# Performance work log

Measured on AMD Instinct MI355X. Metric: run time of the kernel, lower is better.

The kernel has to match this reference:

```python
import jax, jax.numpy as jnp
import numpy as np

N = 50000   # nodes
E = 800000  # edges
R = 2000    # relations
F = 128     # node_F / rel_F
DEPTH = 2
FD = F * (DEPTH + 1)  # 384
P = 64      # proxy rows
EPS = 1e-12


def setup_inputs() -> dict:
    key = jax.random.key(0)
    ks = jax.random.split(key, 16)
    inp = {
        'ent_emb': jax.random.normal(ks[0], (N, F), jnp.float32) * 0.05,
        'rel_emb': jax.random.normal(ks[1], (R, F), jnp.float32) * 0.05,
        'edge_src': jax.random.randint(ks[2], (E,), 0, N, jnp.int32),
        'edge_dst': jax.random.randint(ks[3], (E,), 0, N, jnp.int32),
        'edge_rel': jax.random.randint(ks[4], (E,), 0, R, jnp.int32),
        'attn_e': jax.random.normal(ks[5], (DEPTH, F, 1), jnp.float32) * 0.1,
        'gate_e': jax.random.normal(ks[6], (FD, FD), jnp.float32) * 0.05,
        'proxy_e': jax.random.normal(ks[7], (P, FD), jnp.float32) * 0.1,
        'bias_e': jnp.zeros((1, FD), jnp.float32),
        'attn_r': jax.random.normal(ks[8], (DEPTH, F, 1), jnp.float32) * 0.1,
        'gate_r': jax.random.normal(ks[9], (FD, FD), jnp.float32) * 0.05,
        'proxy_r': jax.random.normal(ks[10], (P, FD), jnp.float32) * 0.1,
        'bias_r': jnp.zeros((1, FD), jnp.float32),
    }
    return inp


def _l2norm(x, axis=-1):
    n = jnp.sqrt(jnp.sum(x * x, axis=axis, keepdims=True))
    return x / jnp.maximum(n, EPS)


def _dual(features, rel_emb, edge_src, edge_dst, edge_rel,
          attn_kernels, gate_kernel, proxy, bias):
    feats = jnp.tanh(features)            # [N, F]
    outs = [feats]
    for l in range(DEPTH):
        # per-edge relation feature (mean over relation set == gather here), L2-normalized
        rels_sum = _l2norm(rel_emb[edge_rel])          # [E, F]
        neighs = feats[edge_src]                       # [E, F]
        # Householder reflection of neighbor features across relation direction
        dot = jnp.sum(neighs * rels_sum, axis=1, keepdims=True)
        neighs = neighs - 2.0 * dot * rels_sum
        # edge_softmax normalized by dst
        att1 = jnp.squeeze(rels_sum @ attn_kernels[l], -1)   # [E]
        seg_max = jax.ops.segment_max(att1, edge_dst, num_segments=N)
        ex = jnp.exp(att1 - seg_max[edge_dst])
        seg_sum = jax.ops.segment_sum(ex, edge_dst, num_segments=N)
        att = ex / seg_sum[edge_dst]
        # weighted scatter-sum aggregation
        agg = jax.ops.segment_sum(neighs * att[:, None], edge_dst, num_segments=N)
        feats = jnp.tanh(agg)
        outs.append(feats)
    outputs = jnp.concatenate(outs, axis=1)            # [N, FD]
    proxy_att = jax.nn.softmax(_l2norm(outputs) @ _l2norm(proxy).T, axis=-1)  # [N, P]
    proxy_feature = outputs - proxy_att @ proxy
    gate = jax.nn.sigmoid(proxy_feature @ gate_kernel + bias)
    return gate * outputs + (1.0 - gate) * proxy_feature


def reference(ent_emb, rel_emb, edge_src, edge_dst, edge_rel,
              attn_e, gate_e, proxy_e, bias_e,
              attn_r, gate_r, proxy_r, bias_r):
    # initial features: mean of neighbor entity / relation embeddings per dst node
    deg = jax.ops.segment_sum(jnp.ones((E,), jnp.float32), edge_dst, num_segments=N)
    deg = jnp.maximum(deg, 1.0)[:, None]
    ent_feature = jax.ops.segment_sum(ent_emb[edge_src], edge_dst, num_segments=N) / deg
    rel_feature = jax.ops.segment_sum(rel_emb[edge_rel], edge_dst, num_segments=N) / deg
    out_ent = _dual(ent_feature, rel_emb, edge_src, edge_dst, edge_rel,
                    attn_e, gate_e, proxy_e, bias_e)
    out_rel = _dual(rel_feature, rel_emb, edge_src, edge_dst, edge_rel,
                    attn_r, gate_r, proxy_r, bias_r)
    return jnp.concatenate((out_ent, out_rel), axis=-1)  # [N, 2*FD]
```

## Files before the change

### kernel.cpp

```cpp
#include <hip/hip_runtime.h>
#include <math.h>


#define NN    50000
#define NE    800000
#define NR    2000
#define FF    128
#define FDIM  384
#define OD    768
#define PP    64
#define NEPS  1e-12f
#define NPB   32
#define FSTR  388
#define ASTR  68
#define NBLK  49

typedef unsigned int u32;
typedef unsigned short u16;
typedef __attribute__((ext_vector_type(8))) short bf16x8;
typedef __attribute__((ext_vector_type(8))) _Float16 f16x8;
typedef __attribute__((ext_vector_type(4))) float f32x4;

__device__ int   g_rowptr[NN + 1];
__device__ int   g_cnt[NN];
__device__ int   g_bsum[64];
__device__ u32   g_csr[NE];
__device__ float g_relnorm[NR * FF];
__device__ float2 g_ew[2 * NR];
__device__ __attribute__((aligned(16))) _Float16 g_hh[2][NN][256];
__device__ __attribute__((aligned(16))) _Float16 g_ent16[NN * FF];
__device__ __attribute__((aligned(16))) u16 g_wt_hi[2 * FDIM * FDIM];
__device__ __attribute__((aligned(16))) u16 g_wt_lo[2 * FDIM * FDIM];
__device__ __attribute__((aligned(16))) u16 g_pxn_hi[2 * PP * FDIM];
__device__ __attribute__((aligned(16))) u16 g_pxn_lo[2 * PP * FDIM];
__device__ __attribute__((aligned(16))) u16 g_pxT_hi[2 * FDIM * PP];
__device__ __attribute__((aligned(16))) u16 g_pxT_lo[2 * FDIM * PP];

__device__ __forceinline__ float wsum64(float v) {
#pragma unroll
    for (int m = 32; m > 0; m >>= 1) v += __shfl_xor(v, m, 64);
    return v;
}
__device__ __forceinline__ void red16x2(float& a, float& b) {
#pragma unroll
    for (int m = 1; m < 16; m <<= 1) {
        float ta = __shfl_xor(a, m, 64);
        float tb = __shfl_xor(b, m, 64);
        a += ta; b += tb;
    }
}

__device__ __forceinline__ u32 pack_bf(float f) {
    u32 x = __float_as_uint(f);
    u32 hr = (x + 0x7FFFu + ((x >> 16) & 1u)) & 0xFFFF0000u;
    float res = f - __uint_as_float(hr);
    u32 y = __float_as_uint(res);
    u32 lr = (y + 0x7FFFu + ((y >> 16) & 1u)) >> 16;
    return hr | lr;
}
__device__ __forceinline__ float unpack_bf(u32 pk) {
    return __uint_as_float(pk & 0xFFFF0000u) + __uint_as_float(pk << 16);
}

__device__ __forceinline__ void load_afrag(const u32* p, bf16x8& ah, bf16x8& al) {
    u32 q[8];
    *reinterpret_cast<float4*>(q)     = *reinterpret_cast<const float4*>(p);
    *reinterpret_cast<float4*>(q + 4) = *reinterpret_cast<const float4*>(p + 4);
    union { u32 u[4]; bf16x8 v; } H, L;
#pragma unroll
    for (int j = 0; j < 4; j++) {
        H.u[j] = __builtin_amdgcn_perm(q[2 * j + 1], q[2 * j], 0x07060302u);
        L.u[j] = __builtin_amdgcn_perm(q[2 * j + 1], q[2 * j], 0x05040100u);
    }
    ah = H.v; al = L.v;
}

__global__ __launch_bounds__(256) void k_zero() {
    int i = blockIdx.x * 256 + threadIdx.x;
    if (i < NN) g_cnt[i] = 0;
}

__global__ __launch_bounds__(256) void k_prep_rel(
    const float* __restrict__ rel_emb, const float* __restrict__ attn_e,
    const float* __restrict__ attn_r) {
    int wave = threadIdx.x >> 6, lane = threadIdx.x & 63;
    int r = blockIdx.x * 4 + wave;
    if (r >= NR) return;
    float2 v = *(const float2*)(rel_emb + r * FF + 2 * lane);
    float ss = wsum64(v.x * v.x + v.y * v.y);
    float inv = 1.f / fmaxf(sqrtf(ss), NEPS);
    float rn0 = v.x * inv, rn1 = v.y * inv;
    *(float2*)(g_relnorm + r * FF + 2 * lane) = make_float2(rn0, rn1);
#pragma unroll
    for (int t = 0; t < 4; t++) {
        const float* av = ((t < 2) ? attn_e : attn_r) + (t & 1) * FF + 2 * lane;
        float d = wsum64(rn0 * av[0] + rn1 * av[1]);
        if (lane == 0) ((float*)&g_ew[(t & 1) * NR + r])[t >> 1] = expf(d);
    }
}

__global__ __launch_bounds__(256) void k_prep_ent(const float* __restrict__ ent_emb) {
    int i = (blockIdx.x * 256 + threadIdx.x) * 8;
    if (i >= NN * FF) return;
    float4 a = *(const float4*)(ent_emb + i);
    float4 b = *(const float4*)(ent_emb + i + 4);
    f16x8 h;
    h[0] = (_Float16)a.x; h[1] = (_Float16)a.y; h[2] = (_Float16)a.z; h[3] = (_Float16)a.w;
    h[4] = (_Float16)b.x; h[5] = (_Float16)b.y; h[6] = (_Float16)b.z; h[7] = (_Float16)b.w;
    *(f16x8*)(g_ent16 + i) = h;
}

__global__ __launch_bounds__(256) void k_prep_proxy(
    const float* __restrict__ proxy_e, const float* __restrict__ proxy_r) {
    int wave = threadIdx.x >> 6, lane = threadIdx.x & 63;
    int row = blockIdx.x * 4 + wave;
    if (row >= 2 * PP) return;
    int d = row >> 6, p = row & 63;
    const float* pr = ((d == 0) ? proxy_e : proxy_r) + p * FDIM;
    float v[6];
    float ss = 0.f;
#pragma unroll
    for (int j = 0; j < 6; j++) {
        v[j] = pr[lane + 64 * j];
        ss += v[j] * v[j];
    }
    ss = wsum64(ss);
    float inv = 1.f / fmaxf(sqrtf(ss), NEPS);
#pragma unroll
    for (int j = 0; j < 6; j++) {
        int k = lane + 64 * j;
        u32 pn = pack_bf(v[j] * inv);
        g_pxn_hi[(d * PP + p) * FDIM + k] = (u16)(pn >> 16);
        g_pxn_lo[(d * PP + p) * FDIM + k] = (u16)(pn & 0xFFFFu);
        u32 pt = pack_bf(v[j]);
        g_pxT_hi[(d * FDIM + k) * PP + p] = (u16)(pt >> 16);
        g_pxT_lo[(d * FDIM + k) * PP + p] = (u16)(pt & 0xFFFFu);
    }
}

__global__ __launch_bounds__(256) void k_prep_wt(
    const float* __restrict__ gate_e, const float* __restrict__ gate_r) {
    int idx = blockIdx.x * 256 + threadIdx.x;
    if (idx >= 2 * FDIM * FDIM) return;
    int d = idx / (FDIM * FDIM);
    int rem = idx - d * (FDIM * FDIM);
    int k = rem / FDIM;
    int f = rem - k * FDIM;
    float wv = (d ? gate_r : gate_e)[k * FDIM + f];
    u32 pk = pack_bf(wv);
    g_wt_hi[(d * FDIM + f) * FDIM + k] = (u16)(pk >> 16);
    g_wt_lo[(d * FDIM + f) * FDIM + k] = (u16)(pk & 0xFFFFu);
}

__global__ __launch_bounds__(256) void k_count(const int* __restrict__ dst) {
    int e = blockIdx.x * 256 + threadIdx.x;
    if (e < NE) atomicAdd(&g_cnt[dst[e]], 1);
}

__global__ __launch_bounds__(1024) void k_scan1() {
    __shared__ int s[1024];
    int b = blockIdx.x, tid = threadIdx.x;
    int i = b * 1024 + tid;
    int v = (i < NN) ? g_cnt[i] : 0;
    s[tid] = v;
    __syncthreads();
    for (int off = 1; off < 1024; off <<= 1) {
        int t = (tid >= off) ? s[tid - off] : 0;
        __syncthreads();
        s[tid] += t;
        __syncthreads();
    }
    if (i < NN) {
        g_rowptr[i] = s[tid] - v;
        g_cnt[i] = 0;
    }
    if (tid == 1023) g_bsum[b] = s[1023];
}
__global__ __launch_bounds__(64) void k_scan2() {
    int lane = threadIdx.x;
    int v = (lane < NBLK) ? g_bsum[lane] : 0;
#pragma unroll
    for (int off = 1; off < 64; off <<= 1) {
        int t = __shfl_up(v, off, 64);
        if (lane >= off) v += t;
    }
    if (lane < NBLK) g_bsum[lane] = v;
    if (lane == 0) g_rowptr[NN] = NE;
}
__global__ __launch_bounds__(1024) void k_scan3() {
    int b = blockIdx.x;
    if (b == 0) return;
    int i = b * 1024 + threadIdx.x;
    if (i < NN) g_rowptr[i] += g_bsum[b - 1];
}

__global__ __launch_bounds__(256) void k_fill(
    const int* __restrict__ src, const int* __restrict__ dst,
    const int* __restrict__ rel) {
    int e = blockIdx.x * 256 + threadIdx.x;
    if (e >= NE) return;
    int d = dst[e];
    int pos = atomicAdd(&g_cnt[d], 1);
    g_csr[g_rowptr[d] + pos] = ((u32)src[e] << 16) | (u32)rel[e];
}

__global__ __launch_bounds__(256) void k_init(
    const float* __restrict__ rel_emb, float* __restrict__ out) {
    int wave = threadIdx.x >> 6, lane = threadIdx.x & 63;
    int n = blockIdx.x * 4 + wave;
    if (n >= NN) return;
    int g16 = lane >> 4, li = lane & 15;
    int s0 = g_rowptr[n], s1 = g_rowptr[n + 1];
    float ae[8], ar[8];
#pragma unroll
    for (int i = 0; i < 8; i++) { ae[i] = 0.f; ar[i] = 0.f; }
    for (int idx = s0; idx < s1; idx += 4) {
        int e = idx + g16;
        if (e < s1) {
            u32 pk = g_csr[e];
            int s = (int)(pk >> 16), r = (int)(pk & 0xFFFFu);
            f16x8 ev = *(const f16x8*)(g_ent16 + (size_t)s * FF + 8 * li);
            const float* rp = rel_emb + (size_t)r * FF + 8 * li;
            float4 r0 = *(const float4*)rp, r1 = *(const float4*)(rp + 4);
            float rv[8] = {r0.x, r0.y, r0.z, r0.w, r1.x, r1.y, r1.z, r1.w};
#pragma unroll
            for (int i = 0; i < 8; i++) {
                ae[i] += (float)ev[i];
                ar[i] += rv[i];
            }
        }
    }
#pragma unroll
    for (int mk = 16; mk < 64; mk <<= 1)
#pragma unroll
        for (int i = 0; i < 8; i++) {
            ae[i] += __shfl_xor(ae[i], mk, 64);
            ar[i] += __shfl_xor(ar[i], mk, 64);
        }
    float invd = 1.f / (float)max(s1 - s0, 1);
    if (g16 == 0) {
        float fe[8], fr[8];
#pragma unroll
        for (int i = 0; i < 8; i++) {
            fe[i] = tanhf(ae[i] * invd);
            fr[i] = tanhf(ar[i] * invd);
        }
        float* oe = out + (size_t)n * OD + 8 * li;
        float* orp = out + (size_t)n * OD + FDIM + 8 * li;
        *(float4*)oe = make_float4(fe[0], fe[1], fe[2], fe[3]);
        *(float4*)(oe + 4) = make_float4(fe[4], fe[5], fe[6], fe[7]);
        *(float4*)orp = make_float4(fr[0], fr[1], fr[2], fr[3]);
        *(float4*)(orp + 4) = make_float4(fr[4], fr[5], fr[6], fr[7]);
        _Float16* hh = &g_hh[0][n][0];
        f16x8 he, hr;
#pragma unroll
        for (int i = 0; i < 8; i++) { he[i] = (_Float16)fe[i]; hr[i] = (_Float16)fr[i]; }
        *(f16x8*)(hh + 8 * li) = he;
        *(f16x8*)(hh + 128 + 8 * li) = hr;
    }
}

__global__ __launch_bounds__(256) void k_layer(float* buf, int layer) {
    int wave = threadIdx.x >> 6, lane = threadIdx.x & 63;
    int n = blockIdx.x * 4 + wave;
    if (n >= NN) return;
    int g16 = lane >> 4, li = lane & 15;
    int bo_e = (layer + 1) * FF;
    int bo_r = FDIM + (layer + 1) * FF;
    const float2* ew = g_ew + layer * NR;
    const _Float16* hs = &g_hh[layer][0][0];
    int s0 = g_rowptr[n], s1 = g_rowptr[n + 1];
    if (s1 == s0) {
        if (g16 == 0) {
            float* oe = buf + (size_t)n * OD + bo_e + 8 * li;
            float* orp = buf + (size_t)n * OD + bo_r + 8 * li;
            *(float4*)oe = make_float4(0.f, 0.f, 0.f, 0.f);
            *(float4*)(oe + 4) = make_float4(0.f, 0.f, 0.f, 0.f);
            *(float4*)orp = make_float4(0.f, 0.f, 0.f, 0.f);
            *(float4*)(orp + 4) = make_float4(0.f, 0.f, 0.f, 0.f);
            if (layer == 0) {
                _Float16* hh = &g_hh[1][n][0];
                f16x8 z = (f16x8)(_Float16)0.f;
                *(f16x8*)(hh + 8 * li) = z;
                *(f16x8*)(hh + 128 + 8 * li) = z;
            }
        }
        return;
    }
    float ae[8], ar[8];
#pragma unroll
    for (int i = 0; i < 8; i++) { ae[i] = 0.f; ar[i] = 0.f; }
    float wse = 0.f, wsr = 0.f;
    for (int idx = s0; idx < s1; idx += 4) {
        int e = idx + g16;
        bool act = e < s1;
        u32 pk = g_csr[act ? e : s0];
        int s = (int)(pk >> 16), r = (int)(pk & 0xFFFFu);
        const _Float16* hrow = hs + (size_t)s * 256;
        f16x8 hev = *(const f16x8*)(hrow + 8 * li);
        f16x8 hrv = *(const f16x8*)(hrow + 128 + 8 * li);
        const float* rp = g_relnorm + (size_t)r * FF + 8 * li;
        float4 rn0 = *(const float4*)rp;
        float4 rn1 = *(const float4*)(rp + 4);
        float rnv[8] = {rn0.x, rn0.y, rn0.z, rn0.w, rn1.x, rn1.y, rn1.z, rn1.w};
        float he[8], hr[8];
#pragma unroll
        for (int i = 0; i < 8; i++) { he[i] = (float)hev[i]; hr[i] = (float)hrv[i]; }
        float de = 0.f, dr = 0.f;
#pragma unroll
        for (int i = 0; i < 8; i++) {
            de = fmaf(he[i], rnv[i], de);
            dr = fmaf(hr[i], rnv[i], dr);
        }
        red16x2(de, dr);
        float2 wv = act ? ew[r] : make_float2(0.f, 0.f);
        wse += wv.x; wsr += wv.y;
        float te = -2.f * de, tr = -2.f * dr;
#pragma unroll
        for (int i = 0; i < 8; i++) {
            ae[i] = fmaf(wv.x, fmaf(te, rnv[i], he[i]), ae[i]);
            ar[i] = fmaf(wv.y, fmaf(tr, rnv[i], hr[i]), ar[i]);
        }
    }
#pragma unroll
    for (int mk = 16; mk < 64; mk <<= 1) {
#pragma unroll
        for (int i = 0; i < 8; i++) {
            ae[i] += __shfl_xor(ae[i], mk, 64);
            ar[i] += __shfl_xor(ar[i], mk, 64);
        }
        wse += __shfl_xor(wse, mk, 64);
        wsr += __shfl_xor(wsr, mk, 64);
    }
    float ive = 1.f / wse, ivr = 1.f / wsr;
    if (g16 == 0) {
        float fe[8], fr[8];
#pragma unroll
        for (int i = 0; i < 8; i++) {
            fe[i] = tanhf(ae[i] * ive);
            fr[i] = tanhf(ar[i] * ivr);
        }
        float* oe = buf + (size_t)n * OD + bo_e + 8 * li;
        float* orp = buf + (size_t)n * OD + bo_r + 8 * li;
        *(float4*)oe = make_float4(fe[0], fe[1], fe[2], fe[3]);
        *(float4*)(oe + 4) = make_float4(fe[4], fe[5], fe[6], fe[7]);
        *(float4*)orp = make_float4(fr[0], fr[1], fr[2], fr[3]);
        *(float4*)(orp + 4) = make_float4(fr[4], fr[5], fr[6], fr[7]);
        if (layer == 0) {
            _Float16* hh = &g_hh[1][n][0];
            f16x8 he16, hr16;
#pragma unroll
            for (int i = 0; i < 8; i++) { he16[i] = (_Float16)fe[i]; hr16[i] = (_Float16)fr[i]; }
            *(f16x8*)(hh + 8 * li) = he16;
            *(f16x8*)(hh + 128 + 8 * li) = hr16;
        }
    }
}

__global__ __launch_bounds__(256, 2) void k_pg(
    float* out, const float* __restrict__ bias_e,
    const float* __restrict__ bias_r) {
    __shared__ __attribute__((aligned(16))) u32 o_pk[NPB * FSTR];
    __shared__ __attribute__((aligned(16))) u32 att_pk[NPB * ASTR];
    __shared__ float invn_s[NPB];
    int tid = threadIdx.x;
    int lane = tid & 63, w = tid >> 6;
    int c = lane & 15, kg = lane >> 4;
    int n0 = blockIdx.x * NPB, dual = blockIdx.y;
    int dual_off = dual * FDIM;
    const float* bias = dual ? bias_r : bias_e;
    const u16* wt_h = g_wt_hi + dual * (FDIM * FDIM);
    const u16* wt_l = g_wt_lo + dual * (FDIM * FDIM);
    const u16* pn_h = g_pxn_hi + dual * (PP * FDIM);
    const u16* pn_l = g_pxn_lo + dual * (PP * FDIM);
    const u16* pt_h = g_pxT_hi + dual * (FDIM * PP);
    const u16* pt_l = g_pxT_lo + dual * (FDIM * PP);

    {
        float2 v[8][3];
        float ss[8];
#pragma unroll
        for (int j = 0; j < 8; j++) {
            int n = w + 4 * j;
            int gn = n0 + n;
            if (gn < NN) {
                const float* rp = out + (size_t)gn * OD + dual_off;
#pragma unroll
                for (int q = 0; q < 3; q++) v[j][q] = *(const float2*)(rp + 2 * (lane + 64 * q));
            } else {
                v[j][0] = v[j][1] = v[j][2] = make_float2(0.f, 0.f);
            }
            ss[j] = v[j][0].x * v[j][0].x + v[j][0].y * v[j][0].y
                  + v[j][1].x * v[j][1].x + v[j][1].y * v[j][1].y
                  + v[j][2].x * v[j][2].x + v[j][2].y * v[j][2].y;
        }
#pragma unroll
        for (int m = 32; m > 0; m >>= 1)
#pragma unroll
            for (int j = 0; j < 8; j++) ss[j] += __shfl_xor(ss[j], m, 64);
#pragma unroll
        for (int j = 0; j < 8; j++) {
            int n = w + 4 * j;
            if (lane == 0) invn_s[n] = 1.f / fmaxf(sqrtf(ss[j]), NEPS);
#pragma unroll
            for (int q = 0; q < 3; q++) {
                uint2 pr;
                pr.x = pack_bf(v[j][q].x);
                pr.y = pack_bf(v[j][q].y);
                *(uint2*)(o_pk + n * FSTR + 2 * (lane + 64 * q)) = pr;
            }
        }
    }
    __syncthreads();

    {
        f32x4 lacc[2] = {{0.f,0.f,0.f,0.f},{0.f,0.f,0.f,0.f}};
        const u16* bh_p = pn_h + (16 * w + c) * FDIM;
        const u16* bl_p = pn_l + (16 * w + c) * FDIM;
#pragma unroll 2
        for (int ks = 0; ks < 12; ks++) {
            int kb = 32 * ks + 8 * kg;
            bf16x8 bh = *(const bf16x8*)(bh_p + kb);
            bf16x8 bl = *(const bf16x8*)(bl_p + kb);
#pragma unroll
            for (int m = 0; m < 2; m++) {
                bf16x8 ah, al;
                load_afrag(o_pk + (16 * m + c) * FSTR + kb, ah, al);
                lacc[m] = __builtin_amdgcn_mfma_f32_16x16x32_bf16(ah, bh, lacc[m], 0, 0, 0);
                lacc[m] = __builtin_amdgcn_mfma_f32_16x16x32_bf16(al, bh, lacc[m], 0, 0, 0);
                lacc[m] = __builtin_amdgcn_mfma_f32_16x16x32_bf16(ah, bl, lacc[m], 0, 0, 0);
            }
        }
#pragma unroll
        for (int m = 0; m < 2; m++)
#pragma unroll
            for (int i = 0; i < 4; i++) {
                int n = 16 * m + 4 * kg + i;
                att_pk[n * ASTR + 16 * w + c] = __float_as_uint(lacc[m][i] * invn_s[n]);
            }
    }
    __syncthreads();

    {
        float ev[8], sv[8];
#pragma unroll
        for (int j = 0; j < 8; j++) {
            int n = w + 4 * j;
            ev[j] = expf(__uint_as_float(att_pk[n * ASTR + lane]));
            sv[j] = ev[j];
        }
#pragma unroll
        for (int m = 32; m > 0; m >>= 1)
#pragma unroll
            for (int j = 0; j < 8; j++) sv[j] += __shfl_xor(sv[j], m, 64);
#pragma unroll
        for (int j = 0; j < 8; j++) {
            int n = w + 4 * j;
            att_pk[n * ASTR + lane] = pack_bf(ev[j] / sv[j]);
        }
    }
    __syncthreads();

    f32x4 pacc[2][6];
#pragma unroll
    for (int m = 0; m < 2; m++)
#pragma unroll
        for (int t = 0; t < 6; t++) pacc[m][t] = (f32x4){0.f, 0.f, 0.f, 0.f};
    {
        bf16x8 aah[2][2], aal[2][2];
#pragma unroll
        for (int m = 0; m < 2; m++) {
            load_afrag(att_pk + (16 * m + c) * ASTR + 8 * kg, aah[m][0], aal[m][0]);
            load_afrag(att_pk + (16 * m + c) * ASTR + 32 + 8 * kg, aah[m][1], aal[m][1]);
        }
#pragma unroll
        for (int t = 0; t < 6; t++) {
            int f = 96 * w + 16 * t + c;
            const u16* bh0 = pt_h + f * PP;
            const u16* bl0 = pt_l + f * PP;
            bf16x8 b0h = *(const bf16x8*)(bh0 + 8 * kg);
            bf16x8 b0l = *(const bf16x8*)(bl0 + 8 * kg);
            bf16x8 b1h = *(const bf16x8*)(bh0 + 32 + 8 * kg);
            bf16x8 b1l = *(const bf16x8*)(bl0 + 32 + 8 * kg);
#pragma unroll
            for (int m = 0; m < 2; m++) {
                pacc[m][t] = __builtin_amdgcn_mfma_f32_16x16x32_bf16(aah[m][0], b0h, pacc[m][t], 0, 0, 0);
                pacc[m][t] = __builtin_amdgcn_mfma_f32_16x16x32_bf16(aal[m][0], b0h, pacc[m][t], 0, 0, 0);
                pacc[m][t] = __builtin_amdgcn_mfma_f32_16x16x32_bf16(aah[m][0], b0l, pacc[m][t], 0, 0, 0);
                pacc[m][t] = __builtin_amdgcn_mfma_f32_16x16x32_bf16(aah[m][1], b1h, pacc[m][t], 0, 0, 0);
                pacc[m][t] = __builtin_amdgcn_mfma_f32_16x16x32_bf16(aal[m][1], b1h, pacc[m][t], 0, 0, 0);
                pacc[m][t] = __builtin_amdgcn_mfma_f32_16x16x32_bf16(aah[m][1], b1l, pacc[m][t], 0, 0, 0);
            }
        }
#pragma unroll
        for (int t = 0; t < 6; t++) {
            int f = 96 * w + 16 * t + c;
#pragma unroll
            for (int m = 0; m < 2; m++)
#pragma unroll
                for (int i = 0; i < 4; i++) {
                    int n = 16 * m + 4 * kg + i;
                    u32 pk = o_pk[n * FSTR + f];
                    o_pk[n * FSTR + f] = pack_bf(unpack_bf(pk) - pacc[m][t][i]);
                }
        }
    }
    __syncthreads();

    f32x4 gacc[2][6];
#pragma unroll
    for (int m = 0; m < 2; m++)
#pragma unroll
        for (int t = 0; t < 6; t++) gacc[m][t] = (f32x4){0.f, 0.f, 0.f, 0.f};
    {
        const u16* wtw_h = wt_h + (96 * w + c) * FDIM;
        const u16* wtw_l = wt_l + (96 * w + c) * FDIM;
#pragma unroll 2
        for (int ks = 0; ks < 12; ks++) {
            int kb = 32 * ks + 8 * kg;
            bf16x8 bhv[6], blv[6];
#pragma unroll
            for (int t = 0; t < 6; t++) {
                bhv[t] = *(const bf16x8*)(wtw_h + t * 16 * FDIM + kb);
                blv[t] = *(const bf16x8*)(wtw_l + t * 16 * FDIM + kb);
            }
            bf16x8 ah[2], al[2];
#pragma unroll
            for (int m = 0; m < 2; m++)
                load_afrag(o_pk + (16 * m + c) * FSTR + kb, ah[m], al[m]);
#pragma unroll
            for (int t = 0; t < 6; t++)
#pragma unroll
                for (int m = 0; m < 2; m++) {
                    gacc[m][t] = __builtin_amdgcn_mfma_f32_16x16x32_bf16(ah[m], bhv[t], gacc[m][t], 0, 0, 0);
                    gacc[m][t] = __builtin_amdgcn_mfma_f32_16x16x32_bf16(al[m], bhv[t], gacc[m][t], 0, 0, 0);
                    gacc[m][t] = __builtin_amdgcn_mfma_f32_16x16x32_bf16(ah[m], blv[t], gacc[m][t], 0, 0, 0);
                }
        }
    }

#pragma unroll
    for (int t = 0; t < 6; t++) {
        int fcol = 96 * w + 16 * t + c;
        float b = bias[fcol];
#pragma unroll
        for (int m = 0; m < 2; m++)
#pragma unroll
            for (int i = 0; i < 4; i++) {
                int n = 16 * m + 4 * kg + i;
                int gn = n0 + n;
                if (gn < NN) {
                    float lin = gacc[m][t][i] + b;
                    float gt = 1.f / (1.f + expf(-lin));
                    float pv = unpack_bf(o_pk[n * FSTR + fcol]);
                    float ov = pv + pacc[m][t][i];
                    out[(size_t)gn * OD + dual_off + fcol] = gt * ov + (1.f - gt) * pv;
                }
            }
    }
}

extern "C" void kernel_launch(void* const* d_in, const int* in_sizes, int n_in,
                              void* d_out, int out_size, void* d_ws, size_t ws_size,
                              hipStream_t stream) {
    const float* ent_emb = (const float*)d_in[0];
    const float* rel_emb = (const float*)d_in[1];
    const int* e_src     = (const int*)d_in[2];
    const int* e_dst     = (const int*)d_in[3];
    const int* e_rel     = (const int*)d_in[4];
    const float* attn_e  = (const float*)d_in[5];
    const float* gate_e  = (const float*)d_in[6];
    const float* proxy_e = (const float*)d_in[7];
    const float* bias_e  = (const float*)d_in[8];
    const float* attn_r  = (const float*)d_in[9];
    const float* gate_r  = (const float*)d_in[10];
    const float* proxy_r = (const float*)d_in[11];
    const float* bias_r  = (const float*)d_in[12];
    float* out = (float*)d_out;
    (void)d_ws; (void)ws_size; (void)in_sizes; (void)n_in; (void)out_size;

    k_zero<<<(NN + 255) / 256, 256, 0, stream>>>();
    k_prep_rel<<<NR / 4, 256, 0, stream>>>(rel_emb, attn_e, attn_r);
    k_prep_ent<<<(NN * FF / 8 + 255) / 256, 256, 0, stream>>>(ent_emb);
    k_prep_proxy<<<32, 256, 0, stream>>>(proxy_e, proxy_r);
    k_prep_wt<<<(2 * FDIM * FDIM + 255) / 256, 256, 0, stream>>>(gate_e, gate_r);
    k_count<<<(NE + 255) / 256, 256, 0, stream>>>(e_dst);
    k_scan1<<<NBLK, 1024, 0, stream>>>();
    k_scan2<<<1, 64, 0, stream>>>();
    k_scan3<<<NBLK, 1024, 0, stream>>>();
    k_fill<<<(NE + 255) / 256, 256, 0, stream>>>(e_src, e_dst, e_rel);
    k_init<<<NN / 4, 256, 0, stream>>>(rel_emb, out);
    k_layer<<<NN / 4, 256, 0, stream>>>(out, 0);
    k_layer<<<NN / 4, 256, 0, stream>>>(out, 1);
    k_pg<<<dim3((NN + NPB - 1) / NPB, 2), 256, 0, stream>>>(out, bias_e, bias_r);
}
```

Baseline: 866.1 us.

## Restructure proxy-gate kernel into independent per-wave 16-row tiles without block barriers

Each wave now processes its own 16 nodes across all 384 output columns, replacing the shared 32-row block tile and its __syncthreads phases with per-wave scratch only. Rows are streamed straight from global memory into MFMA fragments. The row norm and the proxy softmax are done with shuffles inside the wave. The final combine is rewritten algebraically as outputs minus (1-gate) times the proxy term, recomputing the attention-times-proxy product to keep register use down. In exchange, each wave reloads the full gate weight and proxy matrices, doubling weight traffic per row, and register pressure rises sharply from the large accumulator arrays.

Result: slower. 1.885 ms (+117.6%).

```diff
diff --git a/kernel.cpp b/kernel.cpp
--- a/kernel.cpp
+++ b/kernel.cpp
@@ -10,10 +10,9 @@
 #define OD    768
 #define PP    64
 #define NEPS  1e-12f
-#define NPB   32
-#define FSTR  388
-#define ASTR  68
 #define NBLK  49
+#define SCRW  68
+#define TSTR  36
 
 typedef unsigned int u32;
 typedef unsigned short u16;
@@ -62,17 +61,20 @@
     return __uint_as_float(pk & 0xFFFF0000u) + __uint_as_float(pk << 16);
 }
 
+__device__ __forceinline__ void split_frag(const u32 q[8], bf16x8& ah, bf16x8& al) {
+    union { u32 u[4]; bf16x8 v; } H, L;
+#pragma unroll
+    for (int j = 0; j < 4; j++) {
+        H.u[j] = __builtin_amdgcn_perm(q[2 * j + 1], q[2 * j], 0x07060302u);
+        L.u[j] = __builtin_amdgcn_perm(q[2 * j + 1], q[2 * j], 0x05040100u);
+    }
+    ah = H.v; al = L.v;
+}
 __device__ __forceinline__ void load_afrag(const u32* p, bf16x8& ah, bf16x8& al) {
     u32 q[8];
     *reinterpret_cast<float4*>(q)     = *reinterpret_cast<const float4*>(p);
     *reinterpret_cast<float4*>(q + 4) = *reinterpret_cast<const float4*>(p + 4);
-    union { u32 u[4]; bf16x8 v; } H, L;
-#pragma unroll
-    for (int j = 0; j < 4; j++) {
-        H.u[j] = __builtin_amdgcn_perm(q[2 * j + 1], q[2 * j], 0x07060302u);
-        L.u[j] = __builtin_amdgcn_perm(q[2 * j + 1], q[2 * j], 0x05040100u);
-    }
-    ah = H.v; al = L.v;
+    split_frag(q, ah, al);
 }
 
 __global__ __launch_bounds__(256) void k_zero() {
@@ -360,14 +362,14 @@
 __global__ __launch_bounds__(256, 2) void k_pg(
     float* out, const float* __restrict__ bias_e,
     const float* __restrict__ bias_r) {
-    __shared__ __attribute__((aligned(16))) u32 o_pk[NPB * FSTR];
-    __shared__ __attribute__((aligned(16))) u32 att_pk[NPB * ASTR];
-    __shared__ float invn_s[NPB];
+    __shared__ __attribute__((aligned(16))) u32 scr[4][16 * SCRW + 16 * TSTR];
     int tid = threadIdx.x;
     int lane = tid & 63, w = tid >> 6;
     int c = lane & 15, kg = lane >> 4;
-    int n0 = blockIdx.x * NPB, dual = blockIdx.y;
-    int dual_off = dual * FDIM;
+    int dual = blockIdx.y;
+    int n0w = blockIdx.x * 64 + w * 16;
+    if (n0w >= NN) return;
+    int doff = dual * FDIM;
     const float* bias = dual ? bias_r : bias_e;
     const u16* wt_h = g_wt_hi + dual * (FDIM * FDIM);
     const u16* wt_l = g_wt_lo + dual * (FDIM * FDIM);
@@ -375,188 +377,157 @@
     const u16* pn_l = g_pxn_lo + dual * (PP * FDIM);
     const u16* pt_h = g_pxT_hi + dual * (FDIM * PP);
     const u16* pt_l = g_pxT_lo + dual * (FDIM * PP);
-
-    {
-        float2 v[8][3];
-        float ss[8];
+    u32* scrA = scr[w];
+    float* scrT = (float*)(scr[w] + 16 * SCRW);
+    const float* orow = out + (size_t)(n0w + c) * OD + doff;
+
+    float ss = 0.f;
+    f32x4 lacc[4];
+#pragma unroll
+    for (int pt = 0; pt < 4; pt++) lacc[pt] = (f32x4){0.f, 0.f, 0.f, 0.f};
+#pragma unroll
+    for (int ks = 0; ks < 12; ks++) {
+        int kb = 32 * ks + 8 * kg;
+        float4 f0 = *(const float4*)(orow + kb);
+        float4 f1 = *(const float4*)(orow + kb + 4);
+        float fv[8] = {f0.x, f0.y, f0.z, f0.w, f1.x, f1.y, f1.z, f1.w};
+        u32 pk[8];
 #pragma unroll
         for (int j = 0; j < 8; j++) {
-            int n = w + 4 * j;
-            int gn = n0 + n;
-            if (gn < NN) {
-                const float* rp = out + (size_t)gn * OD + dual_off;
-#pragma unroll
-                for (int q = 0; q < 3; q++) v[j][q] = *(const float2*)(rp + 2 * (lane + 64 * q));
-            } else {
-                v[j][0] = v[j][1] = v[j][2] = make_float2(0.f, 0.f);
-            }
-            ss[j] = v[j][0].x * v[j][0].x + v[j][0].y * v[j][0].y
-                  + v[j][1].x * v[j][1].x + v[j][1].y * v[j][1].y
-                  + v[j][2].x * v[j][2].x + v[j][2].y * v[j][2].y;
-        }
-#pragma unroll
-        for (int m = 32; m > 0; m >>= 1)
-#pragma unroll
-            for (int j = 0; j < 8; j++) ss[j] += __shfl_xor(ss[j], m, 64);
-#pragma unroll
-        for (int j = 0; j < 8; j++) {
-            int n = w + 4 * j;
-            if (lane == 0) invn_s[n] = 1.f / fmaxf(sqrtf(ss[j]), NEPS);
-#pragma unroll
-            for (int q = 0; q < 3; q++) {
-                uint2 pr;
-                pr.x = pack_bf(v[j][q].x);
-                pr.y = pack_bf(v[j][q].y);
-                *(uint2*)(o_pk + n * FSTR + 2 * (lane + 64 * q)) = pr;
-            }
-        }
-    }
-    __syncthreads();
-
-    {
-        f32x4 lacc[2] = {{0.f,0.f,0.f,0.f},{0.f,0.f,0.f,0.f}};
-        const u16* bh_p = pn_h + (16 * w + c) * FDIM;
-        const u16* bl_p = pn_l + (16 * w + c) * FDIM;
+            ss = fmaf(fv[j], fv[j], ss);
+            pk[j] = pack_bf(fv[j]);
+        }
+        bf16x8 ah, al;
+        split_frag(pk, ah, al);
+#pragma unroll
+        for (int pt = 0; pt < 4; pt++) {
+            bf16x8 bh = *(const bf16x8*)(pn_h + (16 * pt + c) * FDIM + kb);
+            bf16x8 bl = *(const bf16x8*)(pn_l + (16 * pt + c) * FDIM + kb);
+            lacc[pt] = __builtin_amdgcn_mfma_f32_16x16x32_bf16(ah, bh, lacc[pt], 0, 0, 0);
+            lacc[pt] = __builtin_amdgcn_mfma_f32_16x16x32_bf16(al, bh, lacc[pt], 0, 0, 0);
+            lacc[pt] = __builtin_amdgcn_mfma_f32_16x16x32_bf16(ah, bl, lacc[pt], 0, 0, 0);
+        }
+    }
+    ss += __shfl_xor(ss, 16, 64);
+    ss += __shfl_xor(ss, 32, 64);
+    float invn = 1.f / fmaxf(sqrtf(ss), NEPS);
+
+    float ev[4][4], den[4] = {0.f, 0.f, 0.f, 0.f};
+#pragma unroll
+    for (int i = 0; i < 4; i++) {
+        float ivi = __shfl(invn, 4 * kg + i, 64);
+#pragma unroll
+        for (int pt = 0; pt < 4; pt++) {
+            float e = expf(lacc[pt][i] * ivi);
+            ev[pt][i] = e;
+            den[i] += e;
+        }
+    }
+#pragma unroll
+    for (int m = 1; m < 16; m <<= 1)
+#pragma unroll
+        for (int i = 0; i < 4; i++) den[i] += __shfl_xor(den[i], m, 64);
+#pragma unroll
+    for (int i = 0; i < 4; i++) {
+        float rd = 1.f / den[i];
+#pragma unroll
+        for (int pt = 0; pt < 4; pt++)
+            scrA[(4 * kg + i) * SCRW + 16 * pt + c] = pack_bf(ev[pt][i] * rd);
+    }
+    bf16x8 aah0, aal0, aah1, aal1;
+    load_afrag(scrA + c * SCRW + 8 * kg, aah0, aal0);
+    load_afrag(scrA + c * SCRW + 32 + 8 * kg, aah1, aal1);
+
+    f32x4 pacc[24];
+#pragma unroll
+    for (int t = 0; t < 24; t++) pacc[t] = (f32x4){0.f, 0.f, 0.f, 0.f};
 #pragma unroll 2
-        for (int ks = 0; ks < 12; ks++) {
-            int kb = 32 * ks + 8 * kg;
-            bf16x8 bh = *(const bf16x8*)(bh_p + kb);
-            bf16x8 bl = *(const bf16x8*)(bl_p + kb);
-#pragma unroll
-            for (int m = 0; m < 2; m++) {
-                bf16x8 ah, al;
-                load_afrag(o_pk + (16 * m + c) * FSTR + kb, ah, al);
-                lacc[m] = __builtin_amdgcn_mfma_f32_16x16x32_bf16(ah, bh, lacc[m], 0, 0, 0);
-                lacc[m] = __builtin_amdgcn_mfma_f32_16x16x32_bf16(al, bh, lacc[m], 0, 0, 0);
-                lacc[m] = __builtin_amdgcn_mfma_f32_16x16x32_bf16(ah, bl, lacc[m], 0, 0, 0);
-            }
-        }
-#pragma unroll
-        for (int m = 0; m < 2; m++)
-#pragma unroll
-            for (int i = 0; i < 4; i++) {
-                int n = 16 * m + 4 * kg + i;
-                att_pk[n * ASTR + 16 * w + c] = __float_as_uint(lacc[m][i] * invn_s[n]);
-            }
-    }
-    __syncthreads();
-
-    {
-        float ev[8], sv[8];
-#pragma unroll
-        for (int j = 0; j < 8; j++) {
-            int n = w + 4 * j;
-            ev[j] = expf(__uint_as_float(att_pk[n * ASTR + lane]));
-            sv[j] = ev[j];
-        }
-#pragma unroll
-        for (int m = 32; m > 0; m >>= 1)
-#pragma unroll
-            for (int j = 0; j < 8; j++) sv[j] += __shfl_xor(sv[j], m, 64);
-#pragma unroll
-        for (int j = 0; j < 8; j++) {
-            int n = w + 4 * j;
-            att_pk[n * ASTR + lane] = pack_bf(ev[j] / sv[j]);
-        }
-    }
-    __syncthreads();
-
-    f32x4 pacc[2][6];
-#pragma unroll
-    for (int m = 0; m < 2; m++)
-#pragma unroll
-        for (int t = 0; t < 6; t++) pacc[m][t] = (f32x4){0.f, 0.f, 0.f, 0.f};
-    {
-        bf16x8 aah[2][2], aal[2][2];
-#pragma unroll
-        for (int m = 0; m < 2; m++) {
-            load_afrag(att_pk + (16 * m + c) * ASTR + 8 * kg, aah[m][0], aal[m][0]);
-            load_afrag(att_pk + (16 * m + c) * ASTR + 32 + 8 * kg, aah[m][1], aal[m][1]);
-        }
-#pragma unroll
-        for (int t = 0; t < 6; t++) {
-            int f = 96 * w + 16 * t + c;
-            const u16* bh0 = pt_h + f * PP;
-            const u16* bl0 = pt_l + f * PP;
-            bf16x8 b0h = *(const bf16x8*)(bh0 + 8 * kg);
-            bf16x8 b0l = *(const bf16x8*)(bl0 + 8 * kg);
-            bf16x8 b1h = *(const bf16x8*)(bh0 + 32 + 8 * kg);
-            bf16x8 b1l = *(const bf16x8*)(bl0 + 32 + 8 * kg);
-#pragma unroll
-            for (int m = 0; m < 2; m++) {
-                pacc[m][t] = __builtin_amdgcn_mfma_f32_16x16x32_bf16(aah[m][0], b0h, pacc[m][t], 0, 0, 0);
-                pacc[m][t] = __builtin_amdgcn_mfma_f32_16x16x32_bf16(aal[m][0], b0h, pacc[m][t], 0, 0, 0);
-                pacc[m][t] = __builtin_amdgcn_mfma_f32_16x16x32_bf16(aah[m][0], b0l, pacc[m][t], 0, 0, 0);
-                pacc[m][t] = __builtin_amdgcn_mfma_f32_16x16x32_bf16(aah[m][1], b1h, pacc[m][t], 0, 0, 0);
-                pacc[m][t] = __builtin_amdgcn_mfma_f32_16x16x32_bf16(aal[m][1], b1h, pacc[m][t], 0, 0, 0);
-                pacc[m][t] = __builtin_amdgcn_mfma_f32_16x16x32_bf16(aah[m][1], b1l, pacc[m][t], 0, 0, 0);
-            }
-        }
-#pragma unroll
-        for (int t = 0; t < 6; t++) {
-            int f = 96 * w + 16 * t + c;
-#pragma unroll
-            for (int m = 0; m < 2; m++)
-#pragma unroll
-                for (int i = 0; i < 4; i++) {
-                    int n = 16 * m + 4 * kg + i;
-                    u32 pk = o_pk[n * FSTR + f];
-                    o_pk[n * FSTR + f] = pack_bf(unpack_bf(pk) - pacc[m][t][i]);
-                }
-        }
-    }
-    __syncthreads();
-
-    f32x4 gacc[2][6];
-#pragma unroll
-    for (int m = 0; m < 2; m++)
-#pragma unroll
-        for (int t = 0; t < 6; t++) gacc[m][t] = (f32x4){0.f, 0.f, 0.f, 0.f};
-    {
-        const u16* wtw_h = wt_h + (96 * w + c) * FDIM;
-        const u16* wtw_l = wt_l + (96 * w + c) * FDIM;
+    for (int t = 0; t < 24; t++) {
+        const u16* bh0 = pt_h + (16 * t + c) * PP;
+        const u16* bl0 = pt_l + (16 * t + c) * PP;
+        bf16x8 b0h = *(const bf16x8*)(bh0 + 8 * kg);
+        bf16x8 b0l = *(const bf16x8*)(bl0 + 8 * kg);
+        bf16x8 b1h = *(const bf16x8*)(bh0 + 32 + 8 * kg);
+        bf16x8 b1l = *(const bf16x8*)(bl0 + 32 + 8 * kg);
+        pacc[t] = __builtin_amdgcn_mfma_f32_16x16x32_bf16(aah0, b0h, pacc[t], 0, 0, 0);
+        pacc[t] = __builtin_amdgcn_mfma_f32_16x16x32_bf16(aal0, b0h, pacc[t], 0, 0, 0);
+        pacc[t] = __builtin_amdgcn_mfma_f32_16x16x32_bf16(aah0, b0l, pacc[t], 0, 0, 0);
+        pacc[t] = __builtin_amdgcn_mfma_f32_16x16x32_bf16(aah1, b1h, pacc[t], 0, 0, 0);
+        pacc[t] = __builtin_amdgcn_mfma_f32_16x16x32_bf16(aal1, b1h, pacc[t], 0, 0, 0);
+        pacc[t] = __builtin_amdgcn_mfma_f32_16x16x32_bf16(aah1, b1l, pacc[t], 0, 0, 0);
+    }
+
+    bf16x8 pfh[12], pfl[12];
+#pragma unroll
+    for (int ks = 0; ks < 12; ks++) {
+#pragma unroll
+        for (int u = 0; u < 2; u++) {
+            int t = 2 * ks + u;
+#pragma unroll
+            for (int i = 0; i < 4; i++)
+                scrT[(4 * kg + i) * TSTR + 16 * u + c] = pacc[t][i];
+        }
+        int kb = 32 * ks + 8 * kg;
+        float4 o0 = *(const float4*)(orow + kb);
+        float4 o1 = *(const float4*)(orow + kb + 4);
+        float ofv[8] = {o0.x, o0.y, o0.z, o0.w, o1.x, o1.y, o1.z, o1.w};
+        float4 p0 = *(const float4*)(scrT + c * TSTR + 8 * kg);
+        float4 p1 = *(const float4*)(scrT + c * TSTR + 8 * kg + 4);
+        float pfv[8] = {p0.x, p0.y, p0.z, p0.w, p1.x, p1.y, p1.z, p1.w};
+        u32 pk[8];
+#pragma unroll
+        for (int j = 0; j < 8; j++) pk[j] = pack_bf(ofv[j] - pfv[j]);
+        split_frag(pk, pfh[ks], pfl[ks]);
+    }
+
+    f32x4 lin[24];
+#pragma unroll
+    for (int t = 0; t < 24; t++) lin[t] = (f32x4){0.f, 0.f, 0.f, 0.f};
+#pragma unroll
+    for (int ks = 0; ks < 12; ks++) {
+        int kb = 32 * ks + 8 * kg;
+        bf16x8 ah = pfh[ks], al = pfl[ks];
+#pragma unroll 4
+        for (int t = 0; t < 24; t++) {
+            bf16x8 bh = *(const bf16x8*)(wt_h + (16 * t + c) * FDIM + kb);
+            bf16x8 bl = *(const bf16x8*)(wt_l + (16 * t + c) * FDIM + kb);
+            lin[t] = __builtin_amdgcn_mfma_f32_16x16x32_bf16(ah, bh, lin[t], 0, 0, 0);
+            lin[t] = __builtin_amdgcn_mfma_f32_16x16x32_bf16(al, bh, lin[t], 0, 0, 0);
+            lin[t] = __builtin_amdgcn_mfma_f32_16x16x32_bf16(ah, bl, lin[t], 0, 0, 0);
+        }
+    }
+
+    load_afrag(scrA + c * SCRW + 8 * kg, aah0, aal0);
+    load_afrag(scrA + c * SCRW + 32 + 8 * kg, aah1, aal1);
+    f32x4 p2[24];
+#pragma unroll
+    for (int t = 0; t < 24; t++) p2[t] = (f32x4){0.f, 0.f, 0.f, 0.f};
 #pragma unroll 2
-        for (int ks = 0; ks < 12; ks++) {
-            int kb = 32 * ks + 8 * kg;
-            bf16x8 bhv[6], blv[6];
-#pragma unroll
-            for (int t = 0; t < 6; t++) {
-                bhv[t] = *(const bf16x8*)(wtw_h + t * 16 * FDIM + kb);
-                blv[t] = *(const bf16x8*)(wtw_l + t * 16 * FDIM + kb);
-            }
-            bf16x8 ah[2], al[2];
-#pragma unroll
-            for (int m = 0; m < 2; m++)
-                load_afrag(o_pk + (16 * m + c) * FSTR + kb, ah[m], al[m]);
-#pragma unroll
-            for (int t = 0; t < 6; t++)
-#pragma unroll
-                for (int m = 0; m < 2; m++) {
-                    gacc[m][t] = __builtin_amdgcn_mfma_f32_16x16x32_bf16(ah[m], bhv[t], gacc[m][t], 0, 0, 0);
-                    gacc[m][t] = __builtin_amdgcn_mfma_f32_16x16x32_bf16(al[m], bhv[t], gacc[m][t], 0, 0, 0);
-                    gacc[m][t] = __builtin_amdgcn_mfma_f32_16x16x32_bf16(ah[m], blv[t], gacc[m][t], 0, 0, 0);
-                }
-        }
-    }
-
-#pragma unroll
-    for (int t = 0; t < 6; t++) {
-        int fcol = 96 * w + 16 * t + c;
-        float b = bias[fcol];
-#pragma unroll
-        for (int m = 0; m < 2; m++)
-#pragma unroll
-            for (int i = 0; i < 4; i++) {
-                int n = 16 * m + 4 * kg + i;
-                int gn = n0 + n;
-                if (gn < NN) {
-                    float lin = gacc[m][t][i] + b;
-                    float gt = 1.f / (1.f + expf(-lin));
-                    float pv = unpack_bf(o_pk[n * FSTR + fcol]);
-                    float ov = pv + pacc[m][t][i];
-                    out[(size_t)gn * OD + dual_off + fcol] = gt * ov + (1.f - gt) * pv;
-                }
-            }
+    for (int t = 0; t < 24; t++) {
+        const u16* bh0 = pt_h + (16 * t + c) * PP;
+        const u16* bl0 = pt_l + (16 * t + c) * PP;
+        bf16x8 b0h = *(const bf16x8*)(bh0 + 8 * kg);
+        bf16x8 b0l = *(const bf16x8*)(bl0 + 8 * kg);
+        bf16x8 b1h = *(const bf16x8*)(bh0 + 32 + 8 * kg);
+        bf16x8 b1l = *(const bf16x8*)(bl0 + 32 + 8 * kg);
+        p2[t] = __builtin_amdgcn_mfma_f32_16x16x32_bf16(aah0, b0h, p2[t], 0, 0, 0);
+        p2[t] = __builtin_amdgcn_mfma_f32_16x16x32_bf16(aal0, b0h, p2[t], 0, 0, 0);
+        p2[t] = __builtin_amdgcn_mfma_f32_16x16x32_bf16(aah0, b0l, p2[t], 0, 0, 0);
+        p2[t] = __builtin_amdgcn_mfma_f32_16x16x32_bf16(aah1, b1h, p2[t], 0, 0, 0);
+        p2[t] = __builtin_amdgcn_mfma_f32_16x16x32_bf16(aal1, b1h, p2[t], 0, 0, 0);
+        p2[t] = __builtin_amdgcn_mfma_f32_16x16x32_bf16(aah1, b1l, p2[t], 0, 0, 0);
+    }
+#pragma unroll
+    for (int t = 0; t < 24; t++) {
+        float b = bias[16 * t + c];
+#pragma unroll
+        for (int i = 0; i < 4; i++) {
+            float lv = lin[t][i] + b;
+            float gt = 1.f / (1.f + expf(-lv));
+            float* op = out + (size_t)(n0w + 4 * kg + i) * OD + doff + 16 * t + c;
+            float ov = *op;
+            *op = ov - (1.f - gt) * p2[t][i];
+        }
     }
 }
 
@@ -592,5 +563,5 @@
     k_init<<<NN / 4, 256, 0, stream>>>(rel_emb, out);
     k_layer<<<NN / 4, 256, 0, stream>>>(out, 0);
     k_layer<<<NN / 4, 256, 0, stream>>>(out, 1);
-    k_pg<<<dim3((NN + NPB - 1) / NPB, 2), 256, 0, stream>>>(out, bias_e, bias_r);
-}
+    k_pg<<<dim3((NN + 63) / 64, 2), 256, 0, stream>>>(out, bias_e, bias_r);
+}
```
